# Optimization experiments

Hardware: AMD Instinct MI355X
Metric: run time of the kernel (lower is better)

The kernel has to match this reference:

```python
import jax, jax.numpy as jnp
import jax.scipy.linalg
import numpy as np
import math

IMG = 512
PATCH = 14
NDIM = 2
HEAD_DIM = 128  # dim // heads = 4096 // 32
STEPS = math.ceil(IMG / PATCH)  # 37


def setup_inputs() -> dict:
    key = jax.random.key(0)
    k1, = jax.random.split(key, 1)
    gen = jax.random.uniform(k1, (NDIM, 1, HEAD_DIM, HEAD_DIM), dtype=jnp.float32) * (2.0 * math.pi)
    image_sizes = jnp.full((1, NDIM), IMG, dtype=jnp.int32)
    return {"image_sizes": image_sizes, "generator_raw_params": gen}


def _positions():
    # cartesian product of linspace(0,1,STEPS) along each axis -> [1, STEPS**NDIM, NDIM]
    axes = [jnp.linspace(0.0, 1.0, STEPS, dtype=jnp.float32) for _ in range(NDIM)]
    grid = jnp.stack(jnp.meshgrid(*axes, indexing="ij"), axis=-1).reshape(-1, NDIM)
    return grid[None]  # [1, N, NDIM]


def reference(image_sizes, generator_raw_params):
    positions = _positions()  # [1, N, NDIM]; image size is static (512) per jit requirements
    upper = jnp.triu(generator_raw_params, k=1) - 0.5  # [NDIM,1,D,D]
    skew = upper - jnp.swapaxes(upper, -1, -2)          # skew-symmetric bases
    # sum over input dims: generator per position, [1, N, 1, D, D]
    gen_pos = jnp.einsum("bnd,dhij->bnhij", positions, skew)
    cls = jnp.zeros_like(gen_pos[:, :1])                # CLS token generator (identity rotation)
    gen_pos = jnp.concatenate([cls, gen_pos], axis=1)   # [1, N+1, 1, D, D]
    b, n, h, d, _ = gen_pos.shape
    flat = gen_pos.astype(jnp.float32).reshape(b * n * h, d, d)
    rot = jax.vmap(jax.scipy.linalg.expm)(flat)
    return rot.reshape(b, n, h, d, d).astype(positions.dtype)
```

## Files before the change

### kernel.cpp

```cpp
#include <hip/hip_runtime.h>
#include <math.h>

#define STEPS 37
#define NMAT  (STEPS*STEPS + 1)
#define D     128
#define NT    512

typedef _Float16 half8 __attribute__((ext_vector_type(8)));
typedef __fp16   fp16x2 __attribute__((ext_vector_type(2)));
typedef float    f32x4 __attribute__((ext_vector_type(4)));

#define ROWH     136
#define PH_OFF   0
#define PL_OFF   34816
#define QTH_OFF  69632
#define QTL_OFF  104448
#define RED_OFF  139264
#define LDS_BYTES (139264 + 640)

__constant__ float dC[13] = {
    1.0f, 1.0f, 5.0e-1f, 1.6666666666666666e-1f, 4.1666666666666664e-2f,
    8.3333333333333332e-3f, 1.3888888888888889e-3f, 1.9841269841269841e-4f,
    2.4801587301587302e-5f, 2.7557319223985893e-6f, 2.7557319223985888e-7f,
    2.5052108385441720e-8f, 2.0876756987868099e-9f };

template<bool WQT, bool WXR, bool WGL>
__device__ __forceinline__ void matmul_step(unsigned char* sm, float diagc,
                                            float* __restrict__ gout,
                                            int wr, int wc, int lr, int g)
{
    const _Float16* Ah = (const _Float16*)(sm + PH_OFF);
    const _Float16* Al = (const _Float16*)(sm + PL_OFF);
    const _Float16* Bh = (const _Float16*)(sm + QTH_OFF);
    const _Float16* Bl = (const _Float16*)(sm + QTL_OFF);

    f32x4 acc1[4][2] = {};
    f32x4 acc2[4][2] = {};

    #pragma unroll
    for (int ks = 0; ks < 4; ++ks) {
        const int kof = 32*ks + 8*g;
        half8 ah[4], al[4];
        #pragma unroll
        for (int bi = 0; bi < 4; ++bi) {
            const int r = wr*64 + bi*16 + lr;
            ah[bi] = *(const half8*)&Ah[r*ROWH + kof];
            al[bi] = *(const half8*)&Al[r*ROWH + kof];
        }
        #pragma unroll
        for (int bj = 0; bj < 2; ++bj) {
            const int c = wc*32 + bj*16 + lr;
            const half8 qh = *(const half8*)&Bh[c*ROWH + kof];
            const half8 ql = *(const half8*)&Bl[c*ROWH + kof];
            #pragma unroll
            for (int bi = 0; bi < 4; ++bi) {
                acc1[bi][bj] = __builtin_amdgcn_mfma_f32_16x16x32_f16(ah[bi], qh, acc1[bi][bj], 0, 0, 0);
                acc2[bi][bj] = __builtin_amdgcn_mfma_f32_16x16x32_f16(ah[bi], ql, acc2[bi][bj], 0, 0, 0);
                acc2[bi][bj] = __builtin_amdgcn_mfma_f32_16x16x32_f16(al[bi], qh, acc2[bi][bj], 0, 0, 0);
            }
        }
    }

    if (WGL) {
        #pragma unroll
        for (int bi = 0; bi < 4; ++bi)
            #pragma unroll
            for (int bj = 0; bj < 2; ++bj) {
                const int col = wc*32 + bj*16 + lr;
                const int r0  = wr*64 + bi*16 + 4*g;
                #pragma unroll
                for (int q = 0; q < 4; ++q)
                    gout[(r0+q)*D + col] = acc1[bi][bj][q] + acc2[bi][bj][q] * (1.0f/2048.0f);
            }
        return;
    }

    uint2 uhv[4][2], ulv[4][2];
    #pragma unroll
    for (int bi = 0; bi < 4; ++bi) {
        #pragma unroll
        for (int bj = 0; bj < 2; ++bj) {
            const int col = wc*32 + bj*16 + lr;
            const int r0  = wr*64 + bi*16 + 4*g;
            float v[4];
            #pragma unroll
            for (int q = 0; q < 4; ++q)
                v[q] = acc1[bi][bj][q] + acc2[bi][bj][q] * (1.0f/2048.0f);
            if (wr*64 + bi*16 == wc*32 + bj*16) {
                #pragma unroll
                for (int q = 0; q < 4; ++q)
                    if (r0 + q == col) v[q] += diagc;
            }
            const fp16x2 h01 = __builtin_amdgcn_cvt_pkrtz(v[0], v[1]);
            const fp16x2 h23 = __builtin_amdgcn_cvt_pkrtz(v[2], v[3]);
            const fp16x2 l01 = __builtin_amdgcn_cvt_pkrtz((v[0]-(float)h01[0])*2048.f,
                                                          (v[1]-(float)h01[1])*2048.f);
            const fp16x2 l23 = __builtin_amdgcn_cvt_pkrtz((v[2]-(float)h23[0])*2048.f,
                                                          (v[3]-(float)h23[1])*2048.f);
            union { fp16x2 h2[2]; uint2 u; } cvh, cvl;
            cvh.h2[0] = h01; cvh.h2[1] = h23;
            cvl.h2[0] = l01; cvl.h2[1] = l23;
            uhv[bi][bj] = cvh.u; ulv[bi][bj] = cvl.u;
        }
    }
    __syncthreads();

    _Float16* WQh = (_Float16*)(sm + QTH_OFF);
    _Float16* WQl = (_Float16*)(sm + QTL_OFF);
    _Float16* WXh = (_Float16*)(sm + PH_OFF);
    _Float16* WXl = (_Float16*)(sm + PL_OFF);
    #pragma unroll
    for (int bi = 0; bi < 4; ++bi) {
        #pragma unroll
        for (int bj = 0; bj < 2; ++bj) {
            const int col = wc*32 + bj*16 + lr;
            const int r0  = wr*64 + bi*16 + 4*g;
            if (WQT) {
                *(uint2*)&WQh[col*ROWH + r0] = uhv[bi][bj];
                *(uint2*)&WQl[col*ROWH + r0] = ulv[bi][bj];
            }
            if (WXR) {
                union { uint2 u; _Float16 h[4]; } th, tl;
                th.u = uhv[bi][bj]; tl.u = ulv[bi][bj];
                #pragma unroll
                for (int q = 0; q < 4; ++q) {
                    WXh[(r0+q)*ROWH + col] = th.h[q];
                    WXl[(r0+q)*ROWH + col] = tl.h[q];
                }
            }
        }
    }
    __syncthreads();
}

__global__ __launch_bounds__(NT, 1)
void liere_expm_mfma(const float* __restrict__ gen, float* __restrict__ out)
{
    __shared__ __align__(16) unsigned char sm[LDS_BYTES];
    const int tid = threadIdx.x;
    const int wg  = blockIdx.x;

    float px = 0.f, py = 0.f;
    if (wg > 0) {
        const int idx = wg - 1;
        px = (float)(idx / STEPS) * (1.0f/(STEPS-1));
        py = (float)(idx % STEPS) * (1.0f/(STEPS-1));
    }

    float* Gp = (float*)(sm + QTH_OFF);
    const float* g0 = gen;
    const float* g1 = gen + D*D;
    for (int it = 0; it < 32; ++it) {
        const int e = tid + (it << 9);
        const int i = e >> 7, j = e & 127;
        if (i < j) {
            const float v = px*g0[e] + py*g1[e];
            Gp[i*132 + j] =  v;
            Gp[j*132 + i] = -v;
        } else if (i == j) {
            Gp[i*132 + j] = 0.f;
        }
    }
    __syncthreads();

    float* red = (float*)(sm + RED_OFF);
    if (tid < D) {
        float s = 0.f;
        for (int i = 0; i < D; ++i) s += fabsf(Gp[i*132 + tid]);
        red[tid] = s;
    }
    __syncthreads();
    if (tid == 0) {
        float m = 0.f;
        for (int j = 0; j < D; ++j) m = fmaxf(m, red[j]);
        int s = 0;
        if (m > 2.f) s = (int)ceilf(log2f(m)) - 1;
        if (s < 0) s = 0;
        red[128] = (float)s;
        red[129] = exp2f(-(float)s);
    }
    __syncthreads();
    const int   nsq   = (int)red[128];
    const float scale = red[129];

    float vst[32];
    #pragma unroll
    for (int it = 0; it < 32; ++it) {
        const int e = tid + (it << 9);
        vst[it] = Gp[(e>>7)*132 + (e&127)];
    }
    __syncthreads();

    {
        _Float16* Ph = (_Float16*)(sm + PH_OFF);
        _Float16* Pl = (_Float16*)(sm + PL_OFF);
        _Float16* Qh = (_Float16*)(sm + QTH_OFF);
        _Float16* Ql = (_Float16*)(sm + QTL_OFF);
        const float c12 = dC[12], c11 = dC[11];
        #pragma unroll
        for (int it = 0; it < 32; ++it) {
            const int e = tid + (it << 9);
            const int i = e >> 7, j = e & 127;
            const float p = vst[it] * scale;
            const _Float16 ph = (_Float16)p;
            const _Float16 pl = (_Float16)((p - (float)ph) * 2048.f);
            Ph[i*ROWH + j] = ph;
            Pl[i*ROWH + j] = pl;
            const float x = c12*p + ((i == j) ? c11 : 0.f);
            const _Float16 xh = (_Float16)x;
            const _Float16 xl = (_Float16)((x - (float)xh) * 2048.f);
            Qh[j*ROWH + i] = xh;
            Ql[j*ROWH + i] = xl;
        }
    }
    __syncthreads();

    const int lid = tid & 63;
    const int wid = tid >> 6;
    const int wr = wid >> 2, wc = wid & 3;
    const int lr = lid & 15, g = lid >> 4;
    float* gout = out + (size_t)wg * (D*D);

    for (int kk = 10; kk >= 1; --kk)
        matmul_step<true, false, false>(sm, dC[kk], gout, wr, wc, lr, g);
    matmul_step<true, true, false>(sm, dC[0], gout, wr, wc, lr, g);

    if (nsq == 0) {
        const _Float16* Xh = (const _Float16*)(sm + PH_OFF);
        const _Float16* Xl = (const _Float16*)(sm + PL_OFF);
        for (int it = 0; it < 32; ++it) {
            const int e = tid + (it << 9);
            const int i = e >> 7, j = e & 127;
            gout[e] = (float)Xh[i*ROWH + j] + (float)Xl[i*ROWH + j] * (1.0f/2048.0f);
        }
        return;
    }

    for (int t = 0; t < nsq - 1; ++t)
        matmul_step<true, true, false>(sm, 0.f, gout, wr, wc, lr, g);
    matmul_step<false, false, true>(sm, 0.f, gout, wr, wc, lr, g);
}

extern "C" void kernel_launch(void* const* d_in, const int* in_sizes, int n_in,
                              void* d_out, int out_size, void* d_ws, size_t ws_size,
                              hipStream_t stream) {
    (void)in_sizes; (void)n_in; (void)d_ws; (void)ws_size; (void)out_size;
    const float* gen = (const float*)d_in[1];
    float* out = (float*)d_out;
    liere_expm_mfma<<<NMAT, NT, 0, stream>>>(gen, out);
}
```

Baseline: 514.3 us.

## Cut Taylor degree to 7 with stronger scaling, swizzle LDS layout, parallel max-reduce

Lowers the Taylor polynomial from degree 12 to degree 7 and scales the matrix so its norm is at most 0.5 instead of 2, which trades Horner matmuls for extra squarings. Replaces the padded LDS row stride with an XOR-swizzled 256-byte layout so MFMA operand loads avoid bank conflicts without padding. It also vectorizes the column-sum over the symmetric matrix and replaces the single-thread max with a tree reduction. The lower degree with extra squarings may change accuracy relative to the reference.

```diff
diff --git a/kernel.cpp b/kernel.cpp
--- a/kernel.cpp
+++ b/kernel.cpp
@@ -10,48 +10,42 @@
 typedef __fp16   fp16x2 __attribute__((ext_vector_type(2)));
 typedef float    f32x4 __attribute__((ext_vector_type(4)));
 
-#define ROWH     136
 #define PH_OFF   0
-#define PL_OFF   34816
-#define QTH_OFF  69632
-#define QTL_OFF  104448
-#define RED_OFF  139264
-#define LDS_BYTES (139264 + 640)
-
-__constant__ float dC[13] = {
+#define PL_OFF   32768
+#define QTH_OFF  65536
+#define QTL_OFF  98304
+#define RED_OFF  131072
+#define LDS_BYTES (131072 + 640)
+
+__constant__ float dC[8] = {
     1.0f, 1.0f, 5.0e-1f, 1.6666666666666666e-1f, 4.1666666666666664e-2f,
-    8.3333333333333332e-3f, 1.3888888888888889e-3f, 1.9841269841269841e-4f,
-    2.4801587301587302e-5f, 2.7557319223985893e-6f, 2.7557319223985888e-7f,
-    2.5052108385441720e-8f, 2.0876756987868099e-9f };
+    8.3333333333333332e-3f, 1.3888888888888889e-3f, 1.9841269841269841e-4f };
 
 template<bool WQT, bool WXR, bool WGL>
 __device__ __forceinline__ void matmul_step(unsigned char* sm, float diagc,
                                             float* __restrict__ gout,
                                             int wr, int wc, int lr, int g)
 {
-    const _Float16* Ah = (const _Float16*)(sm + PH_OFF);
-    const _Float16* Al = (const _Float16*)(sm + PL_OFF);
-    const _Float16* Bh = (const _Float16*)(sm + QTH_OFF);
-    const _Float16* Bl = (const _Float16*)(sm + QTL_OFF);
-
     f32x4 acc1[4][2] = {};
     f32x4 acc2[4][2] = {};
 
     #pragma unroll
     for (int ks = 0; ks < 4; ++ks) {
-        const int kof = 32*ks + 8*g;
+        const int slot = 4*ks + g;
         half8 ah[4], al[4];
         #pragma unroll
         for (int bi = 0; bi < 4; ++bi) {
             const int r = wr*64 + bi*16 + lr;
-            ah[bi] = *(const half8*)&Ah[r*ROWH + kof];
-            al[bi] = *(const half8*)&Al[r*ROWH + kof];
+            const int off = r*256 + ((slot ^ (r & 7)) << 4);
+            ah[bi] = *(const half8*)(sm + PH_OFF + off);
+            al[bi] = *(const half8*)(sm + PL_OFF + off);
         }
         #pragma unroll
         for (int bj = 0; bj < 2; ++bj) {
             const int c = wc*32 + bj*16 + lr;
-            const half8 qh = *(const half8*)&Bh[c*ROWH + kof];
-            const half8 ql = *(const half8*)&Bl[c*ROWH + kof];
+            const int off = c*256 + ((slot ^ (c & 7)) << 4);
+            const half8 qh = *(const half8*)(sm + QTH_OFF + off);
+            const half8 ql = *(const half8*)(sm + QTL_OFF + off);
             #pragma unroll
             for (int bi = 0; bi < 4; ++bi) {
                 acc1[bi][bj] = __builtin_amdgcn_mfma_f32_16x16x32_f16(ah[bi], qh, acc1[bi][bj], 0, 0, 0);
@@ -105,10 +99,6 @@
     }
     __syncthreads();
 
-    _Float16* WQh = (_Float16*)(sm + QTH_OFF);
-    _Float16* WQl = (_Float16*)(sm + QTL_OFF);
-    _Float16* WXh = (_Float16*)(sm + PH_OFF);
-    _Float16* WXl = (_Float16*)(sm + PL_OFF);
     #pragma unroll
     for (int bi = 0; bi < 4; ++bi) {
         #pragma unroll
@@ -116,16 +106,19 @@
             const int col = wc*32 + bj*16 + lr;
             const int r0  = wr*64 + bi*16 + 4*g;
             if (WQT) {
-                *(uint2*)&WQh[col*ROWH + r0] = uhv[bi][bj];
-                *(uint2*)&WQl[col*ROWH + r0] = ulv[bi][bj];
+                const int off = col*256 + (((r0 >> 3) ^ (col & 7)) << 4) + ((g & 1) << 3);
+                *(uint2*)(sm + QTH_OFF + off) = uhv[bi][bj];
+                *(uint2*)(sm + QTL_OFF + off) = ulv[bi][bj];
             }
             if (WXR) {
                 union { uint2 u; _Float16 h[4]; } th, tl;
                 th.u = uhv[bi][bj]; tl.u = ulv[bi][bj];
                 #pragma unroll
                 for (int q = 0; q < 4; ++q) {
-                    WXh[(r0+q)*ROWH + col] = th.h[q];
-                    WXl[(r0+q)*ROWH + col] = tl.h[q];
+                    const int rr = r0 + q;
+                    const int off = rr*256 + ((((col >> 3) ^ (rr & 7))) << 4) + ((col & 7) << 1);
+                    *(_Float16*)(sm + PH_OFF + off) = th.h[q];
+                    *(_Float16*)(sm + PL_OFF + off) = tl.h[q];
                 }
             }
         }
@@ -147,7 +140,7 @@
         py = (float)(idx % STEPS) * (1.0f/(STEPS-1));
     }
 
-    float* Gp = (float*)(sm + QTH_OFF);
+    float* Gp = (float*)sm;
     const float* g0 = gen;
     const float* g1 = gen + D*D;
     for (int it = 0; it < 32; ++it) {
@@ -166,22 +159,25 @@
     float* red = (float*)(sm + RED_OFF);
     if (tid < D) {
         float s = 0.f;
-        for (int i = 0; i < D; ++i) s += fabsf(Gp[i*132 + tid]);
+        const f32x4* rowp = (const f32x4*)&Gp[tid*132];
+        #pragma unroll 8
+        for (int u = 0; u < 32; ++u) {
+            const f32x4 v = rowp[u];
+            s += fabsf(v.x) + fabsf(v.y) + fabsf(v.z) + fabsf(v.w);
+        }
         red[tid] = s;
     }
     __syncthreads();
-    if (tid == 0) {
-        float m = 0.f;
-        for (int j = 0; j < D; ++j) m = fmaxf(m, red[j]);
-        int s = 0;
-        if (m > 2.f) s = (int)ceilf(log2f(m)) - 1;
-        if (s < 0) s = 0;
-        red[128] = (float)s;
-        red[129] = exp2f(-(float)s);
-    }
-    __syncthreads();
-    const int   nsq   = (int)red[128];
-    const float scale = red[129];
+    #pragma unroll
+    for (int off = 64; off >= 1; off >>= 1) {
+        if (tid < off) red[tid] = fmaxf(red[tid], red[tid + off]);
+        __syncthreads();
+    }
+    const float m = red[0];
+    int nsq = 0;
+    if (m > 0.5f) nsq = (int)ceilf(log2f(m * 2.0f));
+    if (nsq < 0) nsq = 0;
+    const float scale = exp2f(-(float)nsq);
 
     float vst[32];
     #pragma unroll
@@ -192,11 +188,7 @@
     __syncthreads();
 
     {
-        _Float16* Ph = (_Float16*)(sm + PH_OFF);
-        _Float16* Pl = (_Float16*)(sm + PL_OFF);
-        _Float16* Qh = (_Float16*)(sm + QTH_OFF);
-        _Float16* Ql = (_Float16*)(sm + QTL_OFF);
-        const float c12 = dC[12], c11 = dC[11];
+        const float c7 = dC[7], c6 = dC[6];
         #pragma unroll
         for (int it = 0; it < 32; ++it) {
             const int e = tid + (it << 9);
@@ -204,13 +196,15 @@
             const float p = vst[it] * scale;
             const _Float16 ph = (_Float16)p;
             const _Float16 pl = (_Float16)((p - (float)ph) * 2048.f);
-            Ph[i*ROWH + j] = ph;
-            Pl[i*ROWH + j] = pl;
-            const float x = c12*p + ((i == j) ? c11 : 0.f);
+            const int offP = i*256 + (((j >> 3) ^ (i & 7)) << 4) + ((j & 7) << 1);
+            *(_Float16*)(sm + PH_OFF + offP) = ph;
+            *(_Float16*)(sm + PL_OFF + offP) = pl;
+            const float x = c7*p + ((i == j) ? c6 : 0.f);
             const _Float16 xh = (_Float16)x;
             const _Float16 xl = (_Float16)((x - (float)xh) * 2048.f);
-            Qh[j*ROWH + i] = xh;
-            Ql[j*ROWH + i] = xl;
+            const int offQ = j*256 + (((i >> 3) ^ (j & 7)) << 4) + ((i & 7) << 1);
+            *(_Float16*)(sm + QTH_OFF + offQ) = xh;
+            *(_Float16*)(sm + QTL_OFF + offQ) = xl;
         }
     }
     __syncthreads();
@@ -221,17 +215,17 @@
     const int lr = lid & 15, g = lid >> 4;
     float* gout = out + (size_t)wg * (D*D);
 
-    for (int kk = 10; kk >= 1; --kk)
+    for (int kk = 5; kk >= 1; --kk)
         matmul_step<true, false, false>(sm, dC[kk], gout, wr, wc, lr, g);
     matmul_step<true, true, false>(sm, dC[0], gout, wr, wc, lr, g);
 
     if (nsq == 0) {
-        const _Float16* Xh = (const _Float16*)(sm + PH_OFF);
-        const _Float16* Xl = (const _Float16*)(sm + PL_OFF);
         for (int it = 0; it < 32; ++it) {
             const int e = tid + (it << 9);
             const int i = e >> 7, j = e & 127;
-            gout[e] = (float)Xh[i*ROWH + j] + (float)Xl[i*ROWH + j] * (1.0f/2048.0f);
+            const int off = i*256 + (((j >> 3) ^ (i & 7)) << 4) + ((j & 7) << 1);
+            gout[e] = (float)*(_Float16*)(sm + PH_OFF + off)
+                    + (float)*(_Float16*)(sm + PL_OFF + off) * (1.0f/2048.0f);
         }
         return;
     }
```

Result: faster. 465.6 us (-9.5%).
